# Kernel optimization log

Hardware: AMD Instinct MI355X
Metric: run time of the kernel (lower is better)

## Reference

```python
import jax, jax.numpy as jnp
import numpy as np

NUM_HEADS = 16


def _make_rope(n, half_dim, dtype=jnp.float32):
    # standard rotary frequencies: theta = 10000^{-2i/d}
    inv_freq = 1.0 / (10000.0 ** (np.arange(0, half_dim, dtype=np.float32) / half_dim))
    t = np.arange(n, dtype=np.float32)
    ang = np.outer(t, inv_freq)  # [n, half_dim]
    return jnp.asarray(np.cos(ang), dtype), jnp.asarray(np.sin(ang), dtype)


def setup_inputs() -> dict:
    key = jax.random.key(0)
    ks = jax.random.split(key, 10)
    B, N, C = 2, 2048, 1024
    H = NUM_HEADS
    hd = C // H
    q = jax.random.normal(ks[0], (B, N, C), jnp.float32)
    k = jax.random.normal(ks[1], (B, N, C), jnp.float32)
    v = jax.random.normal(ks[2], (B, N, C), jnp.float32)
    cos, sin = _make_rope(N, hd // 2)
    s = 1.0 / np.sqrt(C)
    Wq = jax.random.normal(ks[3], (C, C), jnp.float32) * s
    bq = jax.random.normal(ks[4], (C,), jnp.float32) * 0.02
    Wk = jax.random.normal(ks[5], (C, C), jnp.float32) * s
    bk = jax.random.normal(ks[6], (C,), jnp.float32) * 0.02
    Wv = jax.random.normal(ks[7], (C, C), jnp.float32) * s
    bv = jax.random.normal(ks[8], (C,), jnp.float32) * 0.02
    return {"q": q, "k": k, "v": v,
            "q_cos": cos, "q_sin": sin, "k_cos": cos, "k_sin": sin,
            "Wq": Wq, "bq": bq, "Wk": Wk, "bk": bk, "Wv": Wv, "bv": bv}


def _rope(x, cos, sin):
    # x: [B, H, N, hd]; pairs (x[...,2j], x[...,2j+1]) form complex numbers,
    # rotated by freqs_cis of shape [N, hd//2] (broadcast over B, H).
    xr = x[..., 0::2]
    xi = x[..., 1::2]
    c = cos[None, None]  # [1,1,N,hd//2]
    s = sin[None, None]
    out_r = xr * c - xi * s
    out_i = xr * s + xi * c
    return jnp.stack([out_r, out_i], axis=-1).reshape(x.shape)


def reference(q, k, v, q_cos, q_sin, k_cos, k_sin, Wq, bq, Wk, bk, Wv, bv):
    B, Nq, C = q.shape
    Nk = k.shape[1]
    H = NUM_HEADS
    hd = C // H
    scale = hd ** -0.5
    # QKV projections (torch nn.Linear: x @ W.T + b), split into heads
    qh = (q @ Wq.T + bq).reshape(B, Nq, H, hd).transpose(0, 2, 1, 3)  # [B,H,Nq,hd]
    kh = (k @ Wk.T + bk).reshape(B, Nk, H, hd).transpose(0, 2, 1, 3)
    vh = (v @ Wv.T + bv).reshape(B, Nk, H, hd).transpose(0, 2, 1, 3)
    # inline RoPE on q and k
    qh = _rope(qh, q_cos, q_sin)
    kh = _rope(kh, k_cos, k_sin)
    # scaled dot-product attention (mask=None, dropout=0, non-causal)
    scores = jnp.einsum('bhqd,bhkd->bhqk', qh, kh) * scale
    attn = jax.nn.softmax(scores, axis=-1)
    out = jnp.einsum('bhqk,bhkd->bhqd', attn, vh)
    # merge heads; NOTE: self.proj is never applied in the original forward
    return out.transpose(0, 2, 1, 3).reshape(B, Nq, C)
```

## Files before the change

### kernel.cpp

```cpp
#include <hip/hip_runtime.h>
#include <hip/hip_bf16.h>

typedef float f32x4 __attribute__((ext_vector_type(4)));
typedef float f32x16 __attribute__((ext_vector_type(16)));
typedef short bf16x8 __attribute__((ext_vector_type(8)));

#define NSEQ 2048
#define CDIM 1024
#define NHEAD 16
#define HDIM 64
#define MROWS 4096
#define QSCALE 0.18033688011f
#define DEFER_THR 11.5416f

__device__ __forceinline__ unsigned short f2bf(float f) {
    unsigned int u = __builtin_bit_cast(unsigned int, f);
    u += 0x7FFFu + ((u >> 16) & 1u);
    return (unsigned short)(u >> 16);
}

__device__ __forceinline__ unsigned pkbf(float lo, float hi_) {
    unsigned r;
    asm("v_cvt_pk_bf16_f32 %0, %1, %2" : "=v"(r) : "v"(lo), "v"(hi_));
    return r;
}

__device__ __forceinline__ void gload16(const void* g, void* l) {
    __builtin_amdgcn_global_load_lds(
        (const __attribute__((address_space(1))) unsigned int*)g,
        (__attribute__((address_space(3))) unsigned int*)l, 16, 0, 0);
}

__global__ __launch_bounds__(256) void cvt6_kernel(
    const float* __restrict__ q, const float* __restrict__ k, const float* __restrict__ v,
    const float* __restrict__ wq, const float* __restrict__ wk, const float* __restrict__ wv,
    unsigned short* __restrict__ dq, unsigned short* __restrict__ dk, unsigned short* __restrict__ dv,
    unsigned short* __restrict__ dwq, unsigned short* __restrict__ dwk, unsigned short* __restrict__ dwv)
{
    int b = blockIdx.x;
    const float* s; unsigned short* d; int base;
    if (b < 4096)       { s = q;  d = dq;  base = b; }
    else if (b < 8192)  { s = k;  d = dk;  base = b - 4096; }
    else if (b < 12288) { s = v;  d = dv;  base = b - 8192; }
    else if (b < 13312) { s = wq; d = dwq; base = b - 12288; }
    else if (b < 14336) { s = wk; d = dwk; base = b - 13312; }
    else                { s = wv; d = dwv; base = b - 14336; }
    int i = (base * 256 + threadIdx.x) * 4;
    float4 t4 = *reinterpret_cast<const float4*>(s + i);
    ushort4 o;
    o.x = f2bf(t4.x); o.y = f2bf(t4.y); o.z = f2bf(t4.z); o.w = f2bf(t4.w);
    *reinterpret_cast<ushort4*>(d + i) = o;
}

__global__ __launch_bounds__(256) void gemm_rope_kernel(
    const unsigned short* __restrict__ Xq, const unsigned short* __restrict__ Xk,
    const unsigned short* __restrict__ Xv,
    const unsigned short* __restrict__ Wqb, const unsigned short* __restrict__ Wkb,
    const unsigned short* __restrict__ Wvb,
    const float* __restrict__ bq, const float* __restrict__ bk, const float* __restrict__ bv,
    const float* __restrict__ qcos, const float* __restrict__ qsin,
    const float* __restrict__ kcos, const float* __restrict__ ksin,
    unsigned short* __restrict__ Qh, unsigned short* __restrict__ Kh,
    unsigned short* __restrict__ VT)
{
    __shared__ unsigned short Al[128][72];
    __shared__ unsigned short Bl[128][72];

    const int tid  = threadIdx.x;
    const int wave = tid >> 6;
    const int lane = tid & 63;
    const int lr   = lane & 15;
    const int lg   = lane >> 4;
    const int lk   = lg * 8;
    const int wm   = wave >> 1;
    const int wn   = wave & 1;
    const int m0   = blockIdx.y * 128;
    const int j0   = blockIdx.x * 128;
    const int z    = blockIdx.z;

    const unsigned short* X = (z == 0) ? Xq : (z == 1) ? Xk : Xv;
    const unsigned short* W = (z == 0) ? Wqb : (z == 1) ? Wkb : Wvb;
    const float* bias = (z == 0) ? bq : (z == 1) ? bk : bv;
    const float* cosb = (z == 0) ? qcos : kcos;
    const float* sinb = (z == 0) ? qsin : ksin;

    f32x4 acc[4][4];
    const f32x4 zero4 = {0.f, 0.f, 0.f, 0.f};
    #pragma unroll
    for (int a = 0; a < 4; a++)
        #pragma unroll
        for (int b = 0; b < 4; b++) acc[a][b] = zero4;

    for (int k0 = 0; k0 < CDIM; k0 += 64) {
        __syncthreads();
        #pragma unroll
        for (int it = 0; it < 4; it++) {
            int c = tid + it * 256;
            int row = c >> 3, col = (c & 7) << 3;
            *reinterpret_cast<bf16x8*>(&Al[row][col]) =
                *reinterpret_cast<const bf16x8*>(X + (size_t)(m0 + row) * CDIM + k0 + col);
            *reinterpret_cast<bf16x8*>(&Bl[row][col]) =
                *reinterpret_cast<const bf16x8*>(W + (size_t)(j0 + row) * CDIM + k0 + col);
        }
        __syncthreads();
        #pragma unroll
        for (int ks = 0; ks < 2; ks++) {
            bf16x8 af[4], bfm[4];
            #pragma unroll
            for (int mi = 0; mi < 4; mi++)
                af[mi] = *reinterpret_cast<const bf16x8*>(&Al[wm * 64 + 16 * mi + lr][ks * 32 + lk]);
            #pragma unroll
            for (int ni = 0; ni < 4; ni++)
                bfm[ni] = *reinterpret_cast<const bf16x8*>(&Bl[wn * 64 + 16 * ni + lr][ks * 32 + lk]);
            #pragma unroll
            for (int mi = 0; mi < 4; mi++)
                #pragma unroll
                for (int ni = 0; ni < 4; ni++)
                    acc[mi][ni] = __builtin_amdgcn_mfma_f32_16x16x32_bf16(
                        af[mi], bfm[ni], acc[mi][ni], 0, 0, 0);
        }
    }

    #pragma unroll
    for (int mi = 0; mi < 4; mi++) {
        const int mbase = m0 + wm * 64 + 16 * mi + 4 * lg;
        #pragma unroll
        for (int ni = 0; ni < 4; ni++) {
            const int j  = j0 + wn * 64 + 16 * ni + lr;
            const float bj = bias[j];
            if (z == 2) {
                const int b = mbase >> 11, n = mbase & 2047;
                const int h = j >> 6, d = j & 63;
                ushort4 pk;
                pk.x = f2bf(acc[mi][ni][0] + bj);
                pk.y = f2bf(acc[mi][ni][1] + bj);
                pk.z = f2bf(acc[mi][ni][2] + bj);
                pk.w = f2bf(acc[mi][ni][3] + bj);
                *reinterpret_cast<ushort4*>(VT + ((size_t)((b * NHEAD + h) * HDIM + d) << 11) + n) = pk;
            } else {
                unsigned short* Out = (z == 0) ? Qh : Kh;
                const float scl = (z == 0) ? QSCALE : 1.0f;
                const int hi = (j & 63) >> 1;
                const float sg = (j & 1) ? 1.f : -1.f;
                float vv[4], pp[4];
                #pragma unroll
                for (int r = 0; r < 4; r++) vv[r] = acc[mi][ni][r] + bj;
                #pragma unroll
                for (int r = 0; r < 4; r++) pp[r] = __shfl_xor(vv[r], 1);
                #pragma unroll
                for (int r = 0; r < 4; r++) {
                    const int m = mbase + r;
                    const int b = m >> 11, n = m & 2047;
                    const float c = cosb[n * 32 + hi];
                    const float s = sinb[n * 32 + hi];
                    const float ov = fmaf(vv[r], c, pp[r] * (sg * s)) * scl;
                    Out[((size_t)((b * NHEAD + (j >> 6)) * NSEQ + n) << 6) + (j & 63)] = f2bf(ov);
                }
            }
        }
    }
}

__global__ __launch_bounds__(256, 2) void attn_kernel(
    const unsigned short* __restrict__ Qh, const unsigned short* __restrict__ Kh,
    const unsigned short* __restrict__ VT, float* __restrict__ out,
    float* __restrict__ O2, float2* __restrict__ ML)
{
    __shared__ unsigned char Ksm[2][8192];
    __shared__ unsigned char Vsm[2][8192];

    const int tid  = threadIdx.x;
    const int wave = tid >> 6;
    const int lane = tid & 63;
    const int c    = lane & 31;
    const int hi   = lane >> 5;
    const int bh   = blockIdx.x;
    const int q0w  = blockIdx.y * 128 + wave * 32;
    const int half = blockIdx.z;
    const int kbase = half * 1024;
    const int sw   = (c & 7) << 4;

    const unsigned short* Qb = Qh + (size_t)bh * NSEQ * HDIM;
    const char* Kb = (const char*)(Kh + (size_t)bh * NSEQ * HDIM);
    const char* Vb = (const char*)(VT + (size_t)bh * HDIM * NSEQ);

    bf16x8 qf[4];
    #pragma unroll
    for (int s = 0; s < 4; s++)
        qf[s] = *reinterpret_cast<const bf16x8*>(
            Qb + (size_t)(q0w + c) * HDIM + s * 16 + hi * 8);

    const f32x16 z16 = {0,0,0,0,0,0,0,0,0,0,0,0,0,0,0,0};
    f32x16 o0 = z16, o1 = z16;
    float mrun = -1e30f, lrun = 0.f;

    const int sr7 = lane >> 3;
    const int scb = ((lane & 7) * 16) ^ (sr7 << 4);
    const int ch0 = wave * 2;

    auto stage = [&](int buf, int n0) {
        #pragma unroll
        for (int i = 0; i < 2; ++i) {
            const int row = (ch0 + i) * 8 + sr7;
            gload16(Kb + (size_t)(n0 + row) * 128 + scb, &Ksm[buf][(ch0 + i) * 1024]);
            gload16(Vb + (size_t)row * (NSEQ * 2) + (size_t)n0 * 2 + scb,
                    &Vsm[buf][(ch0 + i) * 1024]);
        }
    };

    stage(0, kbase);
    __syncthreads();
    int cur = 0;

    for (int t = 0; t < 16; ++t) {
        if (t < 15) stage(cur ^ 1, kbase + (t + 1) * 64);

        f32x16 s0 = z16, s1 = z16;
        __builtin_amdgcn_s_setprio(1);
        #pragma unroll
        for (int s = 0; s < 4; s++) {
            const int cb = (32 * s + 16 * hi) ^ sw;
            bf16x8 kf0 = *reinterpret_cast<const bf16x8*>(&Ksm[cur][c * 128 + cb]);
            bf16x8 kf1 = *reinterpret_cast<const bf16x8*>(&Ksm[cur][(32 + c) * 128 + cb]);
            s0 = __builtin_amdgcn_mfma_f32_32x32x16_bf16(kf0, qf[s], s0, 0, 0, 0);
            s1 = __builtin_amdgcn_mfma_f32_32x32x16_bf16(kf1, qf[s], s1, 0, 0, 0);
        }
        __builtin_amdgcn_s_setprio(0);

        float tmx[8];
        #pragma unroll
        for (int i = 0; i < 8; i++)
            tmx[i] = fmaxf(fmaxf(s0[2 * i], s0[2 * i + 1]),
                           fmaxf(s1[2 * i], s1[2 * i + 1]));
        float tm = fmaxf(fmaxf(fmaxf(tmx[0], tmx[1]), fmaxf(tmx[2], tmx[3])),
                         fmaxf(fmaxf(tmx[4], tmx[5]), fmaxf(tmx[6], tmx[7])));
        tm = fmaxf(tm, __shfl_xor(tm, 32));

        if (!__all(tm - mrun <= DEFER_THR)) {
            const float mnew  = fmaxf(mrun, tm);
            const float alpha = exp2f(mrun - mnew);
            mrun = mnew;
            lrun *= alpha;
            #pragma unroll
            for (int r = 0; r < 16; r++) {
                const float ar = __shfl(alpha, (r & 3) + 8 * (r >> 2) + 4 * hi);
                o0[r] *= ar;
                o1[r] *= ar;
            }
        }

        #pragma unroll
        for (int r = 0; r < 16; r++) s0[r] = exp2f(s0[r] - mrun);
        #pragma unroll
        for (int r = 0; r < 16; r++) s1[r] = exp2f(s1[r] - mrun);
        float rsx[8];
        #pragma unroll
        for (int i = 0; i < 8; i++)
            rsx[i] = (s0[2 * i] + s0[2 * i + 1]) + (s1[2 * i] + s1[2 * i + 1]);
        float rs = ((rsx[0] + rsx[1]) + (rsx[2] + rsx[3])) +
                   ((rsx[4] + rsx[5]) + (rsx[6] + rsx[7]));
        rs += __shfl_xor(rs, 32);
        lrun += rs;

        unsigned pw[4][4];
        #pragma unroll
        for (int u = 0; u < 4; u++) {
            const f32x16& sv = (u < 2) ? s0 : s1;
            const int b = (u & 1) * 8;
            unsigned x0 = pkbf(sv[b + 0], sv[b + 1]);
            unsigned y0 = pkbf(sv[b + 4], sv[b + 5]);
            asm("v_permlane32_swap_b32 %0, %1" : "+v"(x0), "+v"(y0));
            unsigned x1 = pkbf(sv[b + 2], sv[b + 3]);
            unsigned y1 = pkbf(sv[b + 6], sv[b + 7]);
            asm("v_permlane32_swap_b32 %0, %1" : "+v"(x1), "+v"(y1));
            pw[u][0] = x0; pw[u][1] = x1; pw[u][2] = y0; pw[u][3] = y1;
        }

        __builtin_amdgcn_s_setprio(1);
        #pragma unroll
        for (int u = 0; u < 4; u++) {
            uint4 w;
            w.x = pw[u][0]; w.y = pw[u][1]; w.z = pw[u][2]; w.w = pw[u][3];
            bf16x8 pa = __builtin_bit_cast(bf16x8, w);
            const int cb = (32 * u + 16 * hi) ^ sw;
            bf16x8 vf0 = *reinterpret_cast<const bf16x8*>(&Vsm[cur][c * 128 + cb]);
            bf16x8 vf1 = *reinterpret_cast<const bf16x8*>(&Vsm[cur][(32 + c) * 128 + cb]);
            o0 = __builtin_amdgcn_mfma_f32_32x32x16_bf16(pa, vf0, o0, 0, 0, 0);
            o1 = __builtin_amdgcn_mfma_f32_32x32x16_bf16(pa, vf1, o1, 0, 0, 0);
        }
        __builtin_amdgcn_s_setprio(0);

        __syncthreads();
        cur ^= 1;
    }

    float* obase = half ? O2 : out;
    const int b = bh >> 4, h = bh & 15;
    #pragma unroll
    for (int r = 0; r < 16; r++) {
        const int qrow = (r & 3) + 8 * (r >> 2) + 4 * hi;
        const int n = q0w + qrow;
        float* op = obase + ((size_t)(b * NSEQ + n) << 10) + h * HDIM + c;
        op[0]  = o0[r];
        op[32] = o1[r];
    }
    if (hi == 0)
        ML[((size_t)half * 32 + bh) * NSEQ + q0w + c] = make_float2(mrun, lrun);
}

__global__ __launch_bounds__(256) void attn_combine(
    float* __restrict__ out, const float* __restrict__ O2,
    const float2* __restrict__ ML)
{
    const int idx4 = blockIdx.x * 256 + threadIdx.x;
    const int e    = idx4 * 4;
    const int row  = e >> 10;
    const int col  = e & 1023;
    const int h    = col >> 6;
    const int b    = row >> 11;
    const int n    = row & 2047;
    const int bh   = b * NHEAD + h;

    const float2 ml1 = ML[(size_t)bh * NSEQ + n];
    const float2 ml2 = ML[((size_t)32 + bh) * NSEQ + n];
    const float M  = fmaxf(ml1.x, ml2.x);
    const float w1 = exp2f(ml1.x - M);
    const float w2 = exp2f(ml2.x - M);
    const float inv = 1.0f / (w1 * ml1.y + w2 * ml2.y);

    float4 a = reinterpret_cast<float4*>(out)[idx4];
    float4 d = reinterpret_cast<const float4*>(O2)[idx4];
    float4 r;
    r.x = (w1 * a.x + w2 * d.x) * inv;
    r.y = (w1 * a.y + w2 * d.y) * inv;
    r.z = (w1 * a.z + w2 * d.z) * inv;
    r.w = (w1 * a.w + w2 * d.w) * inv;
    reinterpret_cast<float4*>(out)[idx4] = r;
}

extern "C" void kernel_launch(void* const* d_in, const int* in_sizes, int n_in,
                              void* d_out, int out_size, void* d_ws, size_t ws_size,
                              hipStream_t stream) {
    const float* q    = (const float*)d_in[0];
    const float* k    = (const float*)d_in[1];
    const float* v    = (const float*)d_in[2];
    const float* qcos = (const float*)d_in[3];
    const float* qsin = (const float*)d_in[4];
    const float* kcos = (const float*)d_in[5];
    const float* ksin = (const float*)d_in[6];
    const float* Wq   = (const float*)d_in[7];
    const float* bq   = (const float*)d_in[8];
    const float* Wk   = (const float*)d_in[9];
    const float* bk   = (const float*)d_in[10];
    const float* Wv   = (const float*)d_in[11];
    const float* bv   = (const float*)d_in[12];
    float* out = (float*)d_out;

    unsigned short* Xqb = (unsigned short*)d_ws;
    unsigned short* Xkb = Xqb + (size_t)MROWS * CDIM;
    unsigned short* Xvb = Xkb + (size_t)MROWS * CDIM;
    unsigned short* Wqb = Xvb + (size_t)MROWS * CDIM;
    unsigned short* Wkb = Wqb + (size_t)CDIM * CDIM;
    unsigned short* Wvb = Wkb + (size_t)CDIM * CDIM;
    unsigned short* Qhb = Wvb + (size_t)CDIM * CDIM;
    unsigned short* Khb = Qhb + (size_t)MROWS * CDIM;
    unsigned short* VTb = Khb + (size_t)MROWS * CDIM;

    float*  O2 = (float*)Xqb;
    float2* ML = (float2*)((char*)d_ws + (size_t)16 * 1024 * 1024);

    cvt6_kernel<<<15360, 256, 0, stream>>>(q, k, v, Wq, Wk, Wv,
                                           Xqb, Xkb, Xvb, Wqb, Wkb, Wvb);

    dim3 gg(CDIM / 128, MROWS / 128, 3);
    gemm_rope_kernel<<<gg, 256, 0, stream>>>(Xqb, Xkb, Xvb, Wqb, Wkb, Wvb,
                                             bq, bk, bv, qcos, qsin, kcos, ksin,
                                             Qhb, Khb, VTb);

    attn_kernel<<<dim3(2 * NHEAD, NSEQ / 128, 2), 256, 0, stream>>>(
        Qhb, Khb, VTb, out, O2, ML);

    attn_combine<<<(MROWS * CDIM / 4) / 256, 256, 0, stream>>>(out, O2, ML);
}
```

Measured before the change: 143.4 us.

## Halve attention K/V tile to 32 keys and raise occupancy to four blocks per CU

The attention kernel now processes 32 keys per iteration instead of 64, halving the K and V shared-memory buffers and the score accumulators per wave. The V tile is relaid out so both d-halves for 32 keys fit in one 4 KB buffer. Launch bounds go from 2 to 4 blocks per CU to exploit the lower LDS and register use. In exchange there are twice as many loop iterations, each with a barrier and an online-softmax max/rescale step, so per-iteration overhead doubles.

```diff
diff --git a/kernel.cpp b/kernel.cpp
--- a/kernel.cpp
+++ b/kernel.cpp
@@ -161,13 +161,13 @@
     }
 }
 
-__global__ __launch_bounds__(256, 2) void attn_kernel(
+__global__ __launch_bounds__(256, 4) void attn_kernel(
     const unsigned short* __restrict__ Qh, const unsigned short* __restrict__ Kh,
     const unsigned short* __restrict__ VT, float* __restrict__ out,
     float* __restrict__ O2, float2* __restrict__ ML)
 {
-    __shared__ unsigned char Ksm[2][8192];
-    __shared__ unsigned char Vsm[2][8192];
+    __shared__ unsigned char Ksm[2][4096];
+    __shared__ unsigned char Vsm[2][4096];
 
     const int tid  = threadIdx.x;
     const int wave = tid >> 6;
@@ -194,44 +194,37 @@
     f32x16 o0 = z16, o1 = z16;
     float mrun = -1e30f, lrun = 0.f;
 
-    const int sr7 = lane >> 3;
-    const int scb = ((lane & 7) * 16) ^ (sr7 << 4);
-    const int ch0 = wave * 2;
+    const int srow = wave * 8 + (lane >> 3);
+    const int lb   = ((lane & 7) * 16) ^ ((srow & 7) << 4);
+    const size_t skoff = (size_t)srow * 128 + lb;
+    const int dv   = (lb & 64) ? (srow + 32) : srow;
+    const size_t svoff = (size_t)dv * (NSEQ * 2) + (lb & 63);
 
     auto stage = [&](int buf, int n0) {
-        #pragma unroll
-        for (int i = 0; i < 2; ++i) {
-            const int row = (ch0 + i) * 8 + sr7;
-            gload16(Kb + (size_t)(n0 + row) * 128 + scb, &Ksm[buf][(ch0 + i) * 1024]);
-            gload16(Vb + (size_t)row * (NSEQ * 2) + (size_t)n0 * 2 + scb,
-                    &Vsm[buf][(ch0 + i) * 1024]);
-        }
+        gload16(Kb + (size_t)n0 * 128 + skoff, &Ksm[buf][wave * 1024]);
+        gload16(Vb + (size_t)n0 * 2 + svoff, &Vsm[buf][wave * 1024]);
     };
 
     stage(0, kbase);
     __syncthreads();
     int cur = 0;
 
-    for (int t = 0; t < 16; ++t) {
-        if (t < 15) stage(cur ^ 1, kbase + (t + 1) * 64);
-
-        f32x16 s0 = z16, s1 = z16;
+    for (int t = 0; t < 32; ++t) {
+        if (t < 31) stage(cur ^ 1, kbase + (t + 1) * 32);
+
+        f32x16 s = z16;
         __builtin_amdgcn_s_setprio(1);
         #pragma unroll
-        for (int s = 0; s < 4; s++) {
-            const int cb = (32 * s + 16 * hi) ^ sw;
-            bf16x8 kf0 = *reinterpret_cast<const bf16x8*>(&Ksm[cur][c * 128 + cb]);
-            bf16x8 kf1 = *reinterpret_cast<const bf16x8*>(&Ksm[cur][(32 + c) * 128 + cb]);
-            s0 = __builtin_amdgcn_mfma_f32_32x32x16_bf16(kf0, qf[s], s0, 0, 0, 0);
-            s1 = __builtin_amdgcn_mfma_f32_32x32x16_bf16(kf1, qf[s], s1, 0, 0, 0);
+        for (int si = 0; si < 4; si++) {
+            bf16x8 kf = *reinterpret_cast<const bf16x8*>(
+                &Ksm[cur][c * 128 + ((si * 32 + hi * 16) ^ sw)]);
+            s = __builtin_amdgcn_mfma_f32_32x32x16_bf16(kf, qf[si], s, 0, 0, 0);
         }
         __builtin_amdgcn_s_setprio(0);
 
         float tmx[8];
         #pragma unroll
-        for (int i = 0; i < 8; i++)
-            tmx[i] = fmaxf(fmaxf(s0[2 * i], s0[2 * i + 1]),
-                           fmaxf(s1[2 * i], s1[2 * i + 1]));
+        for (int i = 0; i < 8; i++) tmx[i] = fmaxf(s[2 * i], s[2 * i + 1]);
         float tm = fmaxf(fmaxf(fmaxf(tmx[0], tmx[1]), fmaxf(tmx[2], tmx[3])),
                          fmaxf(fmaxf(tmx[4], tmx[5]), fmaxf(tmx[6], tmx[7])));
         tm = fmaxf(tm, __shfl_xor(tm, 32));
@@ -250,41 +243,38 @@
         }
 
         #pragma unroll
-        for (int r = 0; r < 16; r++) s0[r] = exp2f(s0[r] - mrun);
-        #pragma unroll
-        for (int r = 0; r < 16; r++) s1[r] = exp2f(s1[r] - mrun);
+        for (int r = 0; r < 16; r++) s[r] = exp2f(s[r] - mrun);
         float rsx[8];
         #pragma unroll
-        for (int i = 0; i < 8; i++)
-            rsx[i] = (s0[2 * i] + s0[2 * i + 1]) + (s1[2 * i] + s1[2 * i + 1]);
+        for (int i = 0; i < 8; i++) rsx[i] = s[2 * i] + s[2 * i + 1];
         float rs = ((rsx[0] + rsx[1]) + (rsx[2] + rsx[3])) +
                    ((rsx[4] + rsx[5]) + (rsx[6] + rsx[7]));
         rs += __shfl_xor(rs, 32);
         lrun += rs;
 
-        unsigned pw[4][4];
-        #pragma unroll
-        for (int u = 0; u < 4; u++) {
-            const f32x16& sv = (u < 2) ? s0 : s1;
-            const int b = (u & 1) * 8;
-            unsigned x0 = pkbf(sv[b + 0], sv[b + 1]);
-            unsigned y0 = pkbf(sv[b + 4], sv[b + 5]);
+        unsigned pw[2][4];
+        #pragma unroll
+        for (int u = 0; u < 2; u++) {
+            const int b = u * 8;
+            unsigned x0 = pkbf(s[b + 0], s[b + 1]);
+            unsigned y0 = pkbf(s[b + 4], s[b + 5]);
             asm("v_permlane32_swap_b32 %0, %1" : "+v"(x0), "+v"(y0));
-            unsigned x1 = pkbf(sv[b + 2], sv[b + 3]);
-            unsigned y1 = pkbf(sv[b + 6], sv[b + 7]);
+            unsigned x1 = pkbf(s[b + 2], s[b + 3]);
+            unsigned y1 = pkbf(s[b + 6], s[b + 7]);
             asm("v_permlane32_swap_b32 %0, %1" : "+v"(x1), "+v"(y1));
             pw[u][0] = x0; pw[u][1] = x1; pw[u][2] = y0; pw[u][3] = y1;
         }
 
         __builtin_amdgcn_s_setprio(1);
         #pragma unroll
-        for (int u = 0; u < 4; u++) {
+        for (int u = 0; u < 2; u++) {
             uint4 w;
             w.x = pw[u][0]; w.y = pw[u][1]; w.z = pw[u][2]; w.w = pw[u][3];
             bf16x8 pa = __builtin_bit_cast(bf16x8, w);
-            const int cb = (32 * u + 16 * hi) ^ sw;
-            bf16x8 vf0 = *reinterpret_cast<const bf16x8*>(&Vsm[cur][c * 128 + cb]);
-            bf16x8 vf1 = *reinterpret_cast<const bf16x8*>(&Vsm[cur][(32 + c) * 128 + cb]);
+            bf16x8 vf0 = *reinterpret_cast<const bf16x8*>(
+                &Vsm[cur][c * 128 + ((u * 32 + hi * 16) ^ sw)]);
+            bf16x8 vf1 = *reinterpret_cast<const bf16x8*>(
+                &Vsm[cur][c * 128 + ((64 + u * 32 + hi * 16) ^ sw)]);
             o0 = __builtin_amdgcn_mfma_f32_32x32x16_bf16(pa, vf0, o0, 0, 0, 0);
             o1 = __builtin_amdgcn_mfma_f32_32x32x16_bf16(pa, vf1, o1, 0, 0, 0);
         }
```

Result: faster. 140.4 us (-2.1%).
